# Optimization experiments

Hardware: AMD Instinct MI355X
Metric: run time of the kernel (lower is better)

Reference implementation:

```python
import jax, jax.numpy as jnp
import numpy as np

N, E, R = 50000, 500000, 3
IN, HID, OUT = 128, 128, 128
NEG_SLOPE = 0.2


def setup_inputs() -> dict:
    key = jax.random.key(0)
    ks = jax.random.split(key, 16)
    g = lambda i, shape: jax.random.normal(ks[i], shape, jnp.float32) * 0.1
    return {
        "x": jax.random.normal(ks[0], (N, IN), jnp.float32),
        "edge_index": jax.random.randint(ks[1], (2, E), 0, N, jnp.int32),
        "edge_type": jax.random.randint(ks[2], (E,), 0, R, jnp.int32),
        "edge_attr": jax.random.normal(ks[3], (E, 1), jnp.float32),
        # conv1 params (RGATConv: per-relation weight, q/k/e attention vectors, edge lin, bias)
        "w1": g(4, (R, IN, HID)), "q1": g(5, (HID, 1)), "k1": g(6, (HID, 1)),
        "le1": g(7, (1, HID)), "e1": g(8, (HID, 1)), "b1": jnp.zeros((HID,), jnp.float32),
        # conv2 params
        "w2": g(9, (R, HID, OUT)), "q2": g(10, (OUT, 1)), "k2": g(11, (OUT, 1)),
        "le2": g(12, (1, OUT)), "e2": g(13, (OUT, 1)), "b2": jnp.zeros((OUT,), jnp.float32),
    }


def _rgat_conv(x, src, dst, edge_type, edge_attr, w, q, k, le, e, b):
    """PyG RGATConv: heads=1, dim=1, additive-self-attention, across-relation softmax."""
    n = x.shape[0]
    # Per-relation linear at node level (equiv. to per-edge bmm with w[edge_type])
    xw = jnp.einsum('ni,rio->rno', x, w)            # [R, N, C]
    x_j = xw[edge_type, src]                          # [E, C] transformed source feats
    x_i = xw[edge_type, dst]                          # [E, C] transformed target feats
    # additive attention logits: q(x_i) + k(x_j) + e(lin_edge(edge_attr))
    alpha = x_i @ q + x_j @ k + (edge_attr @ le) @ e  # [E, 1]
    alpha = jax.nn.leaky_relu(alpha, negative_slope=NEG_SLOPE)
    # across-relation softmax over incoming edges of each target node
    amax = jax.ops.segment_max(alpha, dst, num_segments=n)
    amax = jnp.where(jnp.isfinite(amax), amax, 0.0)   # empty segments -> 0
    ex = jnp.exp(alpha - amax[dst])
    denom = jax.ops.segment_sum(ex, dst, num_segments=n)
    alpha = ex / (denom[dst] + 1e-16)
    # weighted scatter-add aggregation, then bias (concat=True, heads=1)
    out = jax.ops.segment_sum(alpha * x_j, dst, num_segments=n)  # [N, C]
    return out + b


def reference(x, edge_index, edge_type, edge_attr,
              w1, q1, k1, le1, e1, b1,
              w2, q2, k2, le2, e2, b2):
    src, dst = edge_index[0], edge_index[1]
    h = jax.nn.relu(_rgat_conv(x, src, dst, edge_type, edge_attr, w1, q1, k1, le1, e1, b1))
    return _rgat_conv(h, src, dst, edge_type, edge_attr, w2, q2, k2, le2, e2, b2)
```

## Files before the change

### kernel.cpp

```cpp
#include <hip/hip_runtime.h>
#include <hip/hip_bf16.h>
#include <math.h>

typedef __bf16 bf16x8 __attribute__((ext_vector_type(8)));
typedef float f32x4 __attribute__((ext_vector_type(4)));

#define CDIM 128

__global__ void sentinel_kernel(float* outf) {
  if (threadIdx.x == 0) outf[0] = 12345.0f;
}

__global__ __launch_bounds__(256) void prep_kernel(
    const float* __restrict__ w1, const float* __restrict__ w2,
    __hip_bfloat16* __restrict__ wt,
    const float* __restrict__ le1, const float* __restrict__ e1,
    const float* __restrict__ le2, const float* __restrict__ e2,
    float* __restrict__ outc, int* __restrict__ deg, int perW, int n) {
  const int b = blockIdx.x;
  const int tid = threadIdx.x;
  if (b < 48) {
    int t = b * 256 + tid;
    if (t >= perW * 2) return;
    const float* w = (t < perW) ? w1 : w2;
    int tt = (t < perW) ? t : t - perW;
    int r = tt >> 11;
    int rem = tt & 2047;
    int kb = rem >> 7;
    int o = rem & 127;
    const float* wr = w + ((size_t)r << 14);
    union { __hip_bfloat16 h[8]; int4 v; } u;
#pragma unroll
    for (int j = 0; j < 8; ++j)
      u.h[j] = __float2bfloat16(wr[(size_t)(kb * 8 + j) * CDIM + o]);
    *reinterpret_cast<int4*>(wt + (size_t)t * 8) = u.v;
  } else if (b == 48) {
    if (tid < 64) {
      float v1 = le1[tid] * e1[tid] + le1[tid + 64] * e1[tid + 64];
      float v2 = le2[tid] * e2[tid] + le2[tid + 64] * e2[tid + 64];
#pragma unroll
      for (int off = 32; off > 0; off >>= 1) {
        v1 += __shfl_xor(v1, off, 64);
        v2 += __shfl_xor(v2, off, 64);
      }
      if (tid == 0) { outc[0] = v1; outc[1] = v2; }
    }
  } else {
    int i = (b - 49) * 256 + tid;
    if (i < n) deg[i] = 0;
  }
}


__global__ __launch_bounds__(256) void hist_kernel(const int* __restrict__ dstv,
                                                   int* __restrict__ deg, int E) {
  int e = blockIdx.x * 256 + threadIdx.x;
  if (e < E) atomicAdd(&deg[dstv[e]], 1);
}

__global__ __launch_bounds__(256) void scan1_kernel(const int* __restrict__ deg,
                                                    int* __restrict__ rowptr,
                                                    int* __restrict__ partials, int n) {
  __shared__ int sh[256];
  int t = threadIdx.x;
  int base = blockIdx.x * 1024;
  int idx = base + t * 4;
  int v[4]; int s = 0;
#pragma unroll
  for (int j = 0; j < 4; ++j) { v[j] = (idx + j < n) ? deg[idx + j] : 0; s += v[j]; }
  sh[t] = s;
  __syncthreads();
  for (int off = 1; off < 256; off <<= 1) {
    int x = (t >= off) ? sh[t - off] : 0;
    __syncthreads();
    sh[t] += x;
    __syncthreads();
  }
  int excl = sh[t] - s;
  if (t == 255) partials[blockIdx.x] = sh[255];
  int run = excl;
#pragma unroll
  for (int j = 0; j < 4; ++j) {
    if (idx + j < n) rowptr[idx + j] = run;
    run += v[j];
  }
}

__global__ __launch_bounds__(256) void scan2_kernel(int* __restrict__ partials, int nb) {
  __shared__ int sh[256];
  int t = threadIdx.x;
  int v = (t < nb) ? partials[t] : 0;
  sh[t] = v;
  __syncthreads();
  for (int off = 1; off < 256; off <<= 1) {
    int x = (t >= off) ? sh[t - off] : 0;
    __syncthreads();
    sh[t] += x;
    __syncthreads();
  }
  if (t < nb) partials[t] = sh[t] - v;
}

__global__ __launch_bounds__(256) void scan3_kernel(int* __restrict__ rowptr,
                                                    int* __restrict__ cursor,
                                                    const int* __restrict__ partials,
                                                    int n, int E) {
  int i = blockIdx.x * 256 + threadIdx.x;
  if (i < n) {
    int v = rowptr[i] + partials[i >> 10];
    rowptr[i] = v;
    cursor[i] = v;
  } else if (i == n) {
    rowptr[n] = E;
  }
}

__global__ __launch_bounds__(256) void scatter_kernel(
    const int* __restrict__ srcv, const int* __restrict__ dstv,
    const int* __restrict__ etype, const float* __restrict__ eattr,
    int* __restrict__ cursor, int2* __restrict__ kattr, int E, int n) {
  int e = blockIdx.x * 256 + threadIdx.x;
  if (e >= E) return;
  int p = atomicAdd(&cursor[dstv[e]], 1);
  kattr[p] = make_int2(etype[e] * n + srcv[e], __float_as_int(eattr[e]));
}

__global__ __launch_bounds__(256) void gemm_xw_kernel(
    const float* __restrict__ xin, const __hip_bfloat16* __restrict__ wt,
    const float* __restrict__ qv, const float* __restrict__ kv,
    __hip_bfloat16* __restrict__ xwout, float* __restrict__ sq, float* __restrict__ sk,
    int n) {
  __shared__ __hip_bfloat16 wlds[16 * 128 * 8];
  const int base = blockIdx.x * 128;
  const int tid = threadIdx.x;
  const int wave = tid >> 6, lane = tid & 63;
  const int quad = lane >> 4, c16 = lane & 15;

  bf16x8 zf;
#pragma unroll
  for (int j = 0; j < 8; ++j) zf[j] = (__bf16)0.0f;

  bf16x8 af[2][4];
#pragma unroll
  for (int h = 0; h < 2; ++h) {
    int m = base + wave * 32 + h * 16 + c16;
#pragma unroll
    for (int ks = 0; ks < 4; ++ks) {
      if (m < n) {
        const float* xp = xin + (size_t)m * CDIM + ks * 32 + quad * 8;
        f32x4 x0 = *reinterpret_cast<const f32x4*>(xp);
        f32x4 x1 = *reinterpret_cast<const f32x4*>(xp + 4);
        bf16x8 a;
#pragma unroll
        for (int j = 0; j < 4; ++j) { a[j] = (__bf16)x0[j]; a[4 + j] = (__bf16)x1[j]; }
        af[h][ks] = a;
      } else {
        af[h][ks] = zf;
      }
    }
  }

  float qf[8], kf[8];
#pragma unroll
  for (int nt = 0; nt < 8; ++nt) {
    qf[nt] = qv[nt * 16 + c16];
    kf[nt] = kv[nt * 16 + c16];
  }

  for (int r = 0; r < 3; ++r) {
    if (r) __syncthreads();
    {
      const int4* src = reinterpret_cast<const int4*>(wt + ((size_t)r << 14));
      int4* dst = reinterpret_cast<int4*>(wlds);
      for (int i = tid; i < 2048; i += 256) dst[i] = src[i];
    }
    __syncthreads();

    f32x4 acc[2][8];
#pragma unroll
    for (int h = 0; h < 2; ++h)
#pragma unroll
      for (int nt = 0; nt < 8; ++nt) acc[h][nt] = (f32x4){0.f, 0.f, 0.f, 0.f};

#pragma unroll
    for (int ks = 0; ks < 4; ++ks) {
#pragma unroll
      for (int nt = 0; nt < 8; ++nt) {
        bf16x8 b = *reinterpret_cast<const bf16x8*>(
            &wlds[(((ks * 4 + quad) * 128) + nt * 16 + c16) * 8]);
        acc[0][nt] = __builtin_amdgcn_mfma_f32_16x16x32_bf16(af[0][ks], b, acc[0][nt], 0, 0, 0);
        acc[1][nt] = __builtin_amdgcn_mfma_f32_16x16x32_bf16(af[1][ks], b, acc[1][nt], 0, 0, 0);
      }
    }

#pragma unroll
    for (int h = 0; h < 2; ++h) {
      int rowb = base + wave * 32 + h * 16 + quad * 4;
#pragma unroll
      for (int reg = 0; reg < 4; ++reg) {
        int grow = rowb + reg;
        float s_q = 0.f, s_k = 0.f;
#pragma unroll
        for (int nt = 0; nt < 8; ++nt) {
          float v = acc[h][nt][reg];
          if (grow < n)
            xwout[(((size_t)r * n + grow) << 7) + nt * 16 + c16] = __float2bfloat16(v);
          s_q += v * qf[nt];
          s_k += v * kf[nt];
        }
#pragma unroll
        for (int off = 1; off < 16; off <<= 1) {
          s_q += __shfl_xor(s_q, off, 64);
          s_k += __shfl_xor(s_k, off, 64);
        }
        if (c16 == 0 && grow < n) {
          sq[r * n + grow] = s_q;
          sk[r * n + grow] = s_k;
        }
      }
    }
  }
}

__global__ __launch_bounds__(256) void aggregate_kernel(
    const int* __restrict__ rowptr, const int2* __restrict__ kattr,
    const float* __restrict__ sq, const float* __restrict__ sk,
    const __hip_bfloat16* __restrict__ xw, const float* __restrict__ bias,
    const float* __restrict__ cscal, float* __restrict__ out, int n, int do_relu) {
  const int wave = threadIdx.x >> 6, lane = threadIdx.x & 63;
  const int node = blockIdx.x * 4 + wave;
  if (node >= n) return;
  const int g = lane >> 4;
  const int sub = lane & 15;
  const float c = cscal[0];
  const int n2 = n * 2;

  const int start = rowptr[node];
  const int deg = rowptr[node + 1] - start;
  const float s0 = sq[node], s1 = sq[n + node], s2 = sq[n2 + node];

  float acc[8];
#pragma unroll
  for (int t = 0; t < 8; ++t) acc[t] = 0.f;
  float den = 0.f;

  for (int j0 = 0; j0 < deg; j0 += 4) {
    int j = j0 + g;
    if (j < deg) {
      int2 ka = kattr[start + j];
      int kk = ka.x;
      float sv = (kk >= n2) ? s2 : ((kk >= n) ? s1 : s0);
      float l = sv + sk[kk] + c * __int_as_float(ka.y);
      l = l > 0.f ? l : 0.2f * l;
      float w = __expf(l);
      bf16x8 f = *reinterpret_cast<const bf16x8*>(xw + ((size_t)kk << 7) + sub * 8);
#pragma unroll
      for (int t = 0; t < 8; ++t) acc[t] += w * (float)f[t];
      den += w;
    }
  }

#pragma unroll
  for (int t = 0; t < 8; ++t) {
    acc[t] += __shfl_xor(acc[t], 16, 64);
    acc[t] += __shfl_xor(acc[t], 32, 64);
  }
  den += __shfl_xor(den, 16, 64);
  den += __shfl_xor(den, 32, 64);

  if (g == 0) {
    float inv = 1.0f / (den + 1e-16f);
    f32x4 b0 = *reinterpret_cast<const f32x4*>(bias + sub * 8);
    f32x4 b1 = *reinterpret_cast<const f32x4*>(bias + sub * 8 + 4);
    f32x4 o0, o1;
#pragma unroll
    for (int t = 0; t < 4; ++t) {
      o0[t] = acc[t] * inv + b0[t];
      o1[t] = acc[4 + t] * inv + b1[t];
    }
    if (do_relu) {
#pragma unroll
      for (int t = 0; t < 4; ++t) {
        o0[t] = fmaxf(o0[t], 0.f);
        o1[t] = fmaxf(o1[t], 0.f);
      }
    }
    float* op = out + (size_t)node * CDIM + sub * 8;
    *reinterpret_cast<f32x4*>(op) = o0;
    *reinterpret_cast<f32x4*>(op + 4) = o1;
  }
}


extern "C" void kernel_launch(void* const* d_in, const int* in_sizes, int n_in,
                              void* d_out, int out_size, void* d_ws, size_t ws_size,
                              hipStream_t stream) {
  const float* x     = (const float*)d_in[0];
  const int*   eidx  = (const int*)d_in[1];
  const int*   etype = (const int*)d_in[2];
  const float* eattr = (const float*)d_in[3];
  const float* w1  = (const float*)d_in[4];
  const float* q1  = (const float*)d_in[5];
  const float* k1  = (const float*)d_in[6];
  const float* le1 = (const float*)d_in[7];
  const float* e1  = (const float*)d_in[8];
  const float* b1  = (const float*)d_in[9];
  const float* w2  = (const float*)d_in[10];
  const float* q2  = (const float*)d_in[11];
  const float* k2  = (const float*)d_in[12];
  const float* le2 = (const float*)d_in[13];
  const float* e2  = (const float*)d_in[14];
  const float* b2  = (const float*)d_in[15];

  const int N = in_sizes[0] / CDIM;
  const int E = in_sizes[2];
  const int R = in_sizes[4] / (CDIM * CDIM);
  const int* srcv = eidx;
  const int* dstv = eidx + E;

  char* p = (char*)d_ws;
  auto alloc = [&](size_t bytes) -> void* {
    void* q = (void*)p;
    p += (bytes + 255) & ~(size_t)255;
    return q;
  };
  float* sq       = (float*)alloc((size_t)R * N * 4);
  float* sk       = (float*)alloc((size_t)R * N * 4);
  int*   deg      = (int*)alloc((size_t)N * 4);
  int*   rowptr   = (int*)alloc((size_t)(N + 1) * 4);
  int*   cursor   = (int*)alloc((size_t)N * 4);
  int*   partials = (int*)alloc(4096);
  int2*  kattr    = (int2*)alloc((size_t)E * 8);
  __hip_bfloat16* wt = (__hip_bfloat16*)alloc((size_t)2 * R * CDIM * CDIM * 2);
  float* cscal    = (float*)alloc(256);
  __hip_bfloat16* xw = (__hip_bfloat16*)alloc((size_t)R * N * CDIM * 2);

  size_t needed = (size_t)(p - (char*)d_ws);
  if (needed > ws_size) {
    sentinel_kernel<<<1, 64, 0, stream>>>((float*)d_out);
    return;
  }

  float* outp = (float*)d_out;
  float* hbuf = outp;

  const int eg = (E + 255) / 256;
  const int nb = (N + 1023) / 1024;
  const int nodes4 = (N + 3) / 4;
  const int perW = R * 2048;
  const int prep_grid = 49 + (N + 255) / 256;

  prep_kernel<<<prep_grid, 256, 0, stream>>>(w1, w2, wt, le1, e1, le2, e2,
                                             cscal, deg, perW, N);

  hist_kernel<<<eg, 256, 0, stream>>>(dstv, deg, E);
  scan1_kernel<<<nb, 256, 0, stream>>>(deg, rowptr, partials, N);
  scan2_kernel<<<1, 256, 0, stream>>>(partials, nb);
  scan3_kernel<<<(N + 1 + 255) / 256, 256, 0, stream>>>(rowptr, cursor, partials, N, E);
  scatter_kernel<<<eg, 256, 0, stream>>>(srcv, dstv, etype, eattr, cursor, kattr, E, N);

  dim3 ggrid((N + 127) / 128);

  gemm_xw_kernel<<<ggrid, 256, 0, stream>>>(x, wt, q1, k1, xw, sq, sk, N);
  aggregate_kernel<<<nodes4, 256, 0, stream>>>(rowptr, kattr, sq, sk, xw, b1,
                                               cscal + 0, hbuf, N, 1);

  gemm_xw_kernel<<<ggrid, 256, 0, stream>>>(hbuf, wt + (size_t)R * CDIM * CDIM,
                                            q2, k2, xw, sq, sk, N);
  aggregate_kernel<<<nodes4, 256, 0, stream>>>(rowptr, kattr, sq, sk, xw, b2,
                                               cscal + 1, outp, N, 0);
}
```

Baseline: 266.6 us.

## Fuse CSR build launches with decoupled-lookback scan and store hidden layer as bf16

Merges the degree histogram into the weight-prep kernel, replaces the three-kernel scan with one single-pass decoupled-lookback scan, and zeroes the degree and tile-state buffers with a memset. This cuts the launch count in the CSR-build phase. The first layer's output is now written as bf16 into a workspace buffer, so the second GEMM reads half the bytes and skips the fp32-to-bf16 conversion. The lookback scan spins on atomics and relies on earlier tiles having been scheduled, which risks hangs if that ordering does not hold.

```diff
diff --git a/kernel.cpp b/kernel.cpp
--- a/kernel.cpp
+++ b/kernel.cpp
@@ -11,12 +11,13 @@
   if (threadIdx.x == 0) outf[0] = 12345.0f;
 }
 
-__global__ __launch_bounds__(256) void prep_kernel(
+__global__ __launch_bounds__(256) void prep_hist_kernel(
     const float* __restrict__ w1, const float* __restrict__ w2,
     __hip_bfloat16* __restrict__ wt,
     const float* __restrict__ le1, const float* __restrict__ e1,
     const float* __restrict__ le2, const float* __restrict__ e2,
-    float* __restrict__ outc, int* __restrict__ deg, int perW, int n) {
+    float* __restrict__ outc, const int* __restrict__ dstv,
+    int* __restrict__ deg, int perW, int E) {
   const int b = blockIdx.x;
   const int tid = threadIdx.x;
   if (b < 48) {
@@ -46,25 +47,19 @@
       if (tid == 0) { outc[0] = v1; outc[1] = v2; }
     }
   } else {
-    int i = (b - 49) * 256 + tid;
-    if (i < n) deg[i] = 0;
-  }
-}
-
-
-__global__ __launch_bounds__(256) void hist_kernel(const int* __restrict__ dstv,
-                                                   int* __restrict__ deg, int E) {
-  int e = blockIdx.x * 256 + threadIdx.x;
-  if (e < E) atomicAdd(&deg[dstv[e]], 1);
-}
-
-__global__ __launch_bounds__(256) void scan1_kernel(const int* __restrict__ deg,
-                                                    int* __restrict__ rowptr,
-                                                    int* __restrict__ partials, int n) {
+    int e = (b - 49) * 256 + tid;
+    if (e < E) atomicAdd(&deg[dstv[e]], 1);
+  }
+}
+
+__global__ __launch_bounds__(256) void scan_kernel(
+    const int* __restrict__ deg, int* __restrict__ rowptr, int* __restrict__ cursor,
+    int* __restrict__ tstate, int n, int E) {
   __shared__ int sh[256];
-  int t = threadIdx.x;
-  int base = blockIdx.x * 1024;
-  int idx = base + t * 4;
+  __shared__ int shpref;
+  const int tile = blockIdx.x;
+  const int t = threadIdx.x;
+  const int idx = tile * 1024 + t * 4;
   int v[4]; int s = 0;
 #pragma unroll
   for (int j = 0; j < 4; ++j) { v[j] = (idx + j < n) ? deg[idx + j] : 0; s += v[j]; }
@@ -76,43 +71,33 @@
     sh[t] += x;
     __syncthreads();
   }
-  int excl = sh[t] - s;
-  if (t == 255) partials[blockIdx.x] = sh[255];
-  int run = excl;
+  const int excl = sh[t] - s;
+  const int agg = sh[255];
+  if (t == 255)
+    atomicExch(&tstate[tile], (tile == 0) ? ((agg << 2) | 2) : ((agg << 2) | 1));
+  if (t == 0) {
+    int prefix = 0;
+    for (int j = tile - 1; j >= 0;) {
+      int sv = atomicAdd(&tstate[j], 0);
+      int st = sv & 3;
+      if (st == 0) continue;
+      prefix += (sv >> 2);
+      if (st == 2) break;
+      --j;
+    }
+    shpref = prefix;
+  }
+  __syncthreads();
+  const int prefix = shpref;
+  if (t == 255 && tile > 0)
+    atomicExch(&tstate[tile], ((prefix + agg) << 2) | 2);
+  int run = prefix + excl;
 #pragma unroll
   for (int j = 0; j < 4; ++j) {
-    if (idx + j < n) rowptr[idx + j] = run;
+    if (idx + j < n) { rowptr[idx + j] = run; cursor[idx + j] = run; }
     run += v[j];
   }
-}
-
-__global__ __launch_bounds__(256) void scan2_kernel(int* __restrict__ partials, int nb) {
-  __shared__ int sh[256];
-  int t = threadIdx.x;
-  int v = (t < nb) ? partials[t] : 0;
-  sh[t] = v;
-  __syncthreads();
-  for (int off = 1; off < 256; off <<= 1) {
-    int x = (t >= off) ? sh[t - off] : 0;
-    __syncthreads();
-    sh[t] += x;
-    __syncthreads();
-  }
-  if (t < nb) partials[t] = sh[t] - v;
-}
-
-__global__ __launch_bounds__(256) void scan3_kernel(int* __restrict__ rowptr,
-                                                    int* __restrict__ cursor,
-                                                    const int* __restrict__ partials,
-                                                    int n, int E) {
-  int i = blockIdx.x * 256 + threadIdx.x;
-  if (i < n) {
-    int v = rowptr[i] + partials[i >> 10];
-    rowptr[i] = v;
-    cursor[i] = v;
-  } else if (i == n) {
-    rowptr[n] = E;
-  }
+  if (tile == 0 && t == 0) rowptr[n] = E;
 }
 
 __global__ __launch_bounds__(256) void scatter_kernel(
@@ -126,7 +111,8 @@
 }
 
 __global__ __launch_bounds__(256) void gemm_xw_kernel(
-    const float* __restrict__ xin, const __hip_bfloat16* __restrict__ wt,
+    const void* __restrict__ xin, int xin_bf16,
+    const __hip_bfloat16* __restrict__ wt,
     const float* __restrict__ qv, const float* __restrict__ kv,
     __hip_bfloat16* __restrict__ xwout, float* __restrict__ sq, float* __restrict__ sk,
     int n) {
@@ -147,13 +133,18 @@
 #pragma unroll
     for (int ks = 0; ks < 4; ++ks) {
       if (m < n) {
-        const float* xp = xin + (size_t)m * CDIM + ks * 32 + quad * 8;
-        f32x4 x0 = *reinterpret_cast<const f32x4*>(xp);
-        f32x4 x1 = *reinterpret_cast<const f32x4*>(xp + 4);
-        bf16x8 a;
-#pragma unroll
-        for (int j = 0; j < 4; ++j) { a[j] = (__bf16)x0[j]; a[4 + j] = (__bf16)x1[j]; }
-        af[h][ks] = a;
+        size_t off = (size_t)m * CDIM + ks * 32 + quad * 8;
+        if (xin_bf16) {
+          af[h][ks] = *reinterpret_cast<const bf16x8*>((const __hip_bfloat16*)xin + off);
+        } else {
+          const float* xp = (const float*)xin + off;
+          f32x4 x0 = *reinterpret_cast<const f32x4*>(xp);
+          f32x4 x1 = *reinterpret_cast<const f32x4*>(xp + 4);
+          bf16x8 a;
+#pragma unroll
+          for (int j = 0; j < 4; ++j) { a[j] = (__bf16)x0[j]; a[4 + j] = (__bf16)x1[j]; }
+          af[h][ks] = a;
+        }
       } else {
         af[h][ks] = zf;
       }
@@ -226,7 +217,8 @@
     const int* __restrict__ rowptr, const int2* __restrict__ kattr,
     const float* __restrict__ sq, const float* __restrict__ sk,
     const __hip_bfloat16* __restrict__ xw, const float* __restrict__ bias,
-    const float* __restrict__ cscal, float* __restrict__ out, int n, int do_relu) {
+    const float* __restrict__ cscal, void* __restrict__ out, int n,
+    int do_relu, int out_bf16) {
   const int wave = threadIdx.x >> 6, lane = threadIdx.x & 63;
   const int node = blockIdx.x * 4 + wave;
   if (node >= n) return;
@@ -285,9 +277,16 @@
         o1[t] = fmaxf(o1[t], 0.f);
       }
     }
-    float* op = out + (size_t)node * CDIM + sub * 8;
-    *reinterpret_cast<f32x4*>(op) = o0;
-    *reinterpret_cast<f32x4*>(op + 4) = o1;
+    if (out_bf16) {
+      bf16x8 ob;
+#pragma unroll
+      for (int t = 0; t < 4; ++t) { ob[t] = (__bf16)o0[t]; ob[4 + t] = (__bf16)o1[t]; }
+      *reinterpret_cast<bf16x8*>((__hip_bfloat16*)out + (size_t)node * CDIM + sub * 8) = ob;
+    } else {
+      float* op = (float*)out + (size_t)node * CDIM + sub * 8;
+      *reinterpret_cast<f32x4*>(op) = o0;
+      *reinterpret_cast<f32x4*>(op + 4) = o1;
+    }
   }
 }
 
@@ -327,46 +326,47 @@
   float* sq       = (float*)alloc((size_t)R * N * 4);
   float* sk       = (float*)alloc((size_t)R * N * 4);
   int*   deg      = (int*)alloc((size_t)N * 4);
+  int*   tstate   = (int*)alloc(256);
   int*   rowptr   = (int*)alloc((size_t)(N + 1) * 4);
   int*   cursor   = (int*)alloc((size_t)N * 4);
-  int*   partials = (int*)alloc(4096);
   int2*  kattr    = (int2*)alloc((size_t)E * 8);
   __hip_bfloat16* wt = (__hip_bfloat16*)alloc((size_t)2 * R * CDIM * CDIM * 2);
   float* cscal    = (float*)alloc(256);
   __hip_bfloat16* xw = (__hip_bfloat16*)alloc((size_t)R * N * CDIM * 2);
-
-  size_t needed = (size_t)(p - (char*)d_ws);
-  if (needed > ws_size) {
+  size_t base_need = (size_t)(p - (char*)d_ws);
+  __hip_bfloat16* hb = (__hip_bfloat16*)alloc((size_t)N * CDIM * 2);
+  size_t h_need = (size_t)(p - (char*)d_ws);
+
+  if (base_need > ws_size) {
     sentinel_kernel<<<1, 64, 0, stream>>>((float*)d_out);
     return;
   }
+  const int use_bf16_h = (h_need <= ws_size) ? 1 : 0;
 
   float* outp = (float*)d_out;
-  float* hbuf = outp;
+  void* hbuf = use_bf16_h ? (void*)hb : (void*)outp;
 
   const int eg = (E + 255) / 256;
   const int nb = (N + 1023) / 1024;
   const int nodes4 = (N + 3) / 4;
   const int perW = R * 2048;
-  const int prep_grid = 49 + (N + 255) / 256;
-
-  prep_kernel<<<prep_grid, 256, 0, stream>>>(w1, w2, wt, le1, e1, le2, e2,
-                                             cscal, deg, perW, N);
-
-  hist_kernel<<<eg, 256, 0, stream>>>(dstv, deg, E);
-  scan1_kernel<<<nb, 256, 0, stream>>>(deg, rowptr, partials, N);
-  scan2_kernel<<<1, 256, 0, stream>>>(partials, nb);
-  scan3_kernel<<<(N + 1 + 255) / 256, 256, 0, stream>>>(rowptr, cursor, partials, N, E);
+
+  hipMemsetAsync(deg, 0, (size_t)((char*)tstate - (char*)deg) + 256, stream);
+
+  prep_hist_kernel<<<49 + eg, 256, 0, stream>>>(w1, w2, wt, le1, e1, le2, e2,
+                                                cscal, dstv, deg, perW, E);
+  scan_kernel<<<nb, 256, 0, stream>>>(deg, rowptr, cursor, tstate, N, E);
   scatter_kernel<<<eg, 256, 0, stream>>>(srcv, dstv, etype, eattr, cursor, kattr, E, N);
 
   dim3 ggrid((N + 127) / 128);
 
-  gemm_xw_kernel<<<ggrid, 256, 0, stream>>>(x, wt, q1, k1, xw, sq, sk, N);
+  gemm_xw_kernel<<<ggrid, 256, 0, stream>>>(x, 0, wt, q1, k1, xw, sq, sk, N);
   aggregate_kernel<<<nodes4, 256, 0, stream>>>(rowptr, kattr, sq, sk, xw, b1,
-                                               cscal + 0, hbuf, N, 1);
-
-  gemm_xw_kernel<<<ggrid, 256, 0, stream>>>(hbuf, wt + (size_t)R * CDIM * CDIM,
+                                               cscal + 0, hbuf, N, 1, use_bf16_h);
+
+  gemm_xw_kernel<<<ggrid, 256, 0, stream>>>(hbuf, use_bf16_h,
+                                            wt + (size_t)R * CDIM * CDIM,
                                             q2, k2, xw, sq, sk, N);
   aggregate_kernel<<<nodes4, 256, 0, stream>>>(rowptr, kattr, sq, sk, xw, b2,
-                                               cscal + 1, outp, N, 0);
-}
+                                               cscal + 1, outp, N, 0, 0);
+}
```

New measurement: 268.4 us. No clear change (+0.7%).
